# Optimization experiments

Hardware: AMD Instinct MI355X
Metric: run time of the kernel (lower is better)

## Reference

```python
import jax, jax.numpy as jnp
import numpy as np

N, E, P, D = 100000, 800000, 100000, 128

def setup_inputs() -> dict:
    key = jax.random.key(0)
    ks = jax.random.split(key, 24)
    def w(k, i, o):
        return jax.random.normal(k, (i, o), jnp.float32) * (1.0 / np.sqrt(i))
    inp = {
        'x': jax.random.normal(ks[0], (N, D), jnp.float32),
        'src': jax.random.randint(ks[1], (E,), 0, N, jnp.int32),
        'dst': jax.random.randint(ks[2], (E,), 0, N, jnp.int32),
        'pos_src': jax.random.randint(ks[3], (P,), 0, N, jnp.int32),
        'pos_dst': jax.random.randint(ks[4], (P,), 0, N, jnp.int32),
        'neg_src': jax.random.randint(ks[5], (P,), 0, N, jnp.int32),
        'neg_dst': jax.random.randint(ks[6], (P,), 0, N, jnp.int32),
        # SAGEConv params: fc_self, fc_neigh (+bias) per layer
        'Ws0': w(ks[7], D, D), 'Wn0': w(ks[8], D, D), 'b0': jnp.zeros((D,), jnp.float32),
        'Ws1': w(ks[9], D, D), 'Wn1': w(ks[10], D, D), 'b1': jnp.zeros((D,), jnp.float32),
        'Ws2': w(ks[11], D, D), 'Wn2': w(ks[12], D, D), 'b2': jnp.zeros((D,), jnp.float32),
        # predictor MLP: D->D->D->2
        'Wp0': w(ks[13], D, D), 'bp0': jnp.zeros((D,), jnp.float32),
        'Wp1': w(ks[14], D, D), 'bp1': jnp.zeros((D,), jnp.float32),
        'Wp2': w(ks[15], D, 2), 'bp2': jnp.zeros((2,), jnp.float32),
    }
    return inp

def _sage_layer(h, src, dst, n, Ws, Wn, b, act):
    # mean aggregation over in-neighbors (gather -> segment_sum -> divide)
    msum = jax.ops.segment_sum(h[src], dst, num_segments=n)      # [N, D]
    deg = jax.ops.segment_sum(jnp.ones_like(dst, jnp.float32), dst, num_segments=n)
    h_neigh = msum / jnp.maximum(deg, 1.0)[:, None]
    out = h @ Ws + h_neigh @ Wn + b
    return jax.nn.relu(out) if act else out

def _predict(hs, hd, Wp0, bp0, Wp1, bp1, Wp2, bp2):
    z = hs * hd
    z = jax.nn.relu(z @ Wp0 + bp0)
    z = jax.nn.relu(z @ Wp1 + bp1)
    return jax.nn.softmax(z @ Wp2 + bp2, axis=1)[:, 1]

def reference(x, src, dst, pos_src, pos_dst, neg_src, neg_dst,
              Ws0, Wn0, b0, Ws1, Wn1, b1, Ws2, Wn2, b2,
              Wp0, bp0, Wp1, bp1, Wp2, bp2):
    n = x.shape[0]
    h = _sage_layer(x, src, dst, n, Ws0, Wn0, b0, True)
    h = _sage_layer(h, src, dst, n, Ws1, Wn1, b1, True)
    h = _sage_layer(h, src, dst, n, Ws2, Wn2, b2, False)
    pos = _predict(h[pos_src], h[pos_dst], Wp0, bp0, Wp1, bp1, Wp2, bp2)
    neg = _predict(h[neg_src], h[neg_dst], Wp0, bp0, Wp1, bp1, Wp2, bp2)
    return (pos, neg)
```

## Files before the change

### kernel.cpp

```cpp
#include <hip/hip_runtime.h>
#include <cstdint>
#include <cstddef>
#include <cmath>

#define D 128

typedef short bf16x8 __attribute__((ext_vector_type(8)));
typedef float f32x4 __attribute__((ext_vector_type(4)));

__device__ __forceinline__ ushort f2b(float f) {
  uint x = __float_as_uint(f);
  uint r = ((x >> 16) & 1u) + 0x7fffu;
  return (ushort)((x + r) >> 16);
}
__device__ __forceinline__ float b2f(ushort u) {
  return __uint_as_float(((uint)u) << 16);
}

__global__ __launch_bounds__(256) void k_degree_p(const int* __restrict__ dst, int E,
    int* __restrict__ deg, float scale, int CE) {
  int part = blockIdx.x & 7, chunk = blockIdx.x >> 3;
  long base = (long)chunk * CE;
  for (int i = threadIdx.x; i < CE; i += 256) {
    long e = base + i;
    if (e < E) {
      int d = dst[e];
      int p = (int)((float)d * scale); if (p > 7) p = 7;
      if (p == part) atomicAdd(&deg[d], 1);
    }
  }
}

__global__ __launch_bounds__(256) void k_fill_p(const int* __restrict__ src,
    const int* __restrict__ dst, int E, int* __restrict__ cursor,
    int* __restrict__ csrc, float scale, int CE) {
  int part = blockIdx.x & 7, chunk = blockIdx.x >> 3;
  long base = (long)chunk * CE;
  for (int i = threadIdx.x; i < CE; i += 256) {
    long e = base + i;
    if (e < E) {
      int d = dst[e];
      int p = (int)((float)d * scale); if (p > 7) p = 7;
      if (p == part) {
        int s = src[e];
        int pos = atomicAdd(&cursor[d], 1);
        csrc[pos] = s;
      }
    }
  }
}

#define SCAN_T 256
#define SCAN_E 4
#define SCAN_CHUNK (SCAN_T * SCAN_E)

__global__ void k_scan_partial(const int* __restrict__ deg, int n, int* __restrict__ part) {
  __shared__ int s[SCAN_T];
  int base = blockIdx.x * SCAN_CHUNK;
  int sum = 0;
  for (int i = 0; i < SCAN_E; ++i) {
    int idx = base + (int)threadIdx.x * SCAN_E + i;
    if (idx < n) sum += deg[idx];
  }
  s[threadIdx.x] = sum; __syncthreads();
  for (int ofs = SCAN_T / 2; ofs > 0; ofs >>= 1) {
    if ((int)threadIdx.x < ofs) s[threadIdx.x] += s[threadIdx.x + ofs];
    __syncthreads();
  }
  if (threadIdx.x == 0) part[blockIdx.x] = s[0];
}

__global__ void k_scan_part_ex(int* __restrict__ part, int nb) {
  __shared__ int s[1024];
  int v = ((int)threadIdx.x < nb) ? part[threadIdx.x] : 0;
  s[threadIdx.x] = v; __syncthreads();
  for (int ofs = 1; ofs < 1024; ofs <<= 1) {
    int t = ((int)threadIdx.x >= ofs) ? s[threadIdx.x - ofs] : 0;
    __syncthreads();
    s[threadIdx.x] += t;
    __syncthreads();
  }
  if ((int)threadIdx.x < nb) part[threadIdx.x] = s[threadIdx.x] - v;
}

__global__ void k_scan_final(const int* __restrict__ deg, int n, const int* __restrict__ part,
                             int* __restrict__ rowptr, int* __restrict__ cursor, int E) {
  __shared__ int s[SCAN_T];
  int base = blockIdx.x * SCAN_CHUNK;
  int v[SCAN_E]; int local = 0;
  for (int i = 0; i < SCAN_E; ++i) {
    int idx = base + (int)threadIdx.x * SCAN_E + i;
    v[i] = (idx < n) ? deg[idx] : 0;
    local += v[i];
  }
  s[threadIdx.x] = local; __syncthreads();
  for (int ofs = 1; ofs < SCAN_T; ofs <<= 1) {
    int t = ((int)threadIdx.x >= ofs) ? s[threadIdx.x - ofs] : 0;
    __syncthreads();
    s[threadIdx.x] += t;
    __syncthreads();
  }
  int run = part[blockIdx.x] + s[threadIdx.x] - local;
  for (int i = 0; i < SCAN_E; ++i) {
    int idx = base + (int)threadIdx.x * SCAN_E + i;
    if (idx < n) { rowptr[idx] = run; cursor[idx] = run; }
    run += v[i];
  }
  if (blockIdx.x == 0 && threadIdx.x == 0) rowptr[n] = E;
}

__global__ void k_conv_bf16(const float* __restrict__ in, ushort* __restrict__ out, int n8) {
  int i = blockIdx.x * 256 + threadIdx.x;
  if (i >= n8) return;
  float4 a = ((const float4*)in)[i * 2];
  float4 b = ((const float4*)in)[i * 2 + 1];
  ushort4 o0 = {f2b(a.x), f2b(a.y), f2b(a.z), f2b(a.w)};
  ushort4 o1 = {f2b(b.x), f2b(b.y), f2b(b.z), f2b(b.w)};
  ((ushort4*)out)[i * 2] = o0;
  ((ushort4*)out)[i * 2 + 1] = o1;
}

__global__ void k_pack_all(
    const float* __restrict__ Ws0, const float* __restrict__ Wn0,
    const float* __restrict__ Ws1, const float* __restrict__ Wn1,
    const float* __restrict__ Ws2, const float* __restrict__ Wn2,
    const float* __restrict__ Wp0, const float* __restrict__ Wp1,
    ushort* __restrict__ BpL0, ushort* __restrict__ BpL1, ushort* __restrict__ BpL2,
    ushort* __restrict__ BpP0, ushort* __restrict__ BpP1) {
  int o = blockIdx.x * 256 + threadIdx.x;
  const float *W0, *W1; ushort* out; int rel;
  if (o < 32768)       { W0 = Ws0; W1 = Wn0; out = BpL0; rel = o; }
  else if (o < 65536)  { W0 = Ws1; W1 = Wn1; out = BpL1; rel = o - 32768; }
  else if (o < 98304)  { W0 = Ws2; W1 = Wn2; out = BpL2; rel = o - 65536; }
  else if (o < 114688) { W0 = Wp0; W1 = Wp0; out = BpP0; rel = o - 98304; }
  else                 { W0 = Wp1; W1 = Wp1; out = BpP1; rel = o - 114688; }
  int j = rel & 7, lane = (rel >> 3) & 63, t = (rel >> 9) & 7, ks = rel >> 12;
  int k = ks * 32 + ((lane >> 4) * 8) + j;
  int n = t * 16 + (lane & 15);
  const float* W = (k < 128) ? W0 : W1;
  int kk = (k < 128) ? k : k - 128;
  out[rel] = f2b(W[(size_t)kk * D + n]);
}

#define SMS 136
__global__ __launch_bounds__(256) void k_sage_fused(
    const ushort* __restrict__ A, const int* __restrict__ rowptr,
    const int* __restrict__ csrc, const ushort* __restrict__ Bp,
    const float* __restrict__ bias, ushort* __restrict__ out, int N, int do_relu) {
  __shared__ __align__(16) ushort smean[64][SMS];
  int tid = threadIdx.x, wave = tid >> 6, lane = tid & 63;
  int m = lane & 15, kg = lane >> 4;
  int g = tid >> 4, sub = tid & 15;
  const ushort* hb = A + sub * 8;
  #pragma unroll
  for (int j = 0; j < 4; ++j) {
    int r = g * 4 + j;
    int node = blockIdx.x * 64 + r;
    int beg = 0, end = 0;
    if (node < N) { beg = rowptr[node]; end = rowptr[node + 1]; }
    float f[8] = {0.f, 0.f, 0.f, 0.f, 0.f, 0.f, 0.f, 0.f};
    int i = beg;
    for (; i + 3 < end; i += 4) {
      int s0 = csrc[i], s1 = csrc[i + 1], s2 = csrc[i + 2], s3 = csrc[i + 3];
      bf16x8 v0 = *(const bf16x8*)(hb + (size_t)s0 * D);
      bf16x8 v1 = *(const bf16x8*)(hb + (size_t)s1 * D);
      bf16x8 v2 = *(const bf16x8*)(hb + (size_t)s2 * D);
      bf16x8 v3 = *(const bf16x8*)(hb + (size_t)s3 * D);
      #pragma unroll
      for (int q = 0; q < 8; ++q)
        f[q] += (b2f((ushort)v0[q]) + b2f((ushort)v1[q]))
              + (b2f((ushort)v2[q]) + b2f((ushort)v3[q]));
    }
    for (; i < end; ++i) {
      int s0 = csrc[i];
      bf16x8 v0 = *(const bf16x8*)(hb + (size_t)s0 * D);
      #pragma unroll
      for (int q = 0; q < 8; ++q) f[q] += b2f((ushort)v0[q]);
    }
    float inv = (end > beg) ? (1.0f / (float)(end - beg)) : 0.0f;
    bf16x8 o;
    #pragma unroll
    for (int q = 0; q < 8; ++q) o[q] = (short)f2b(f[q] * inv);
    *(bf16x8*)&smean[r][sub * 8] = o;
  }
  __syncthreads();
  int row0 = blockIdx.x * 64 + wave * 16;
  int ar = row0 + m; if (ar >= N) ar = N - 1;
  const ushort* a_self = A + (size_t)ar * D + kg * 8;
  f32x4 acc[8];
  #pragma unroll
  for (int t = 0; t < 8; ++t) acc[t] = f32x4{0.f, 0.f, 0.f, 0.f};
  #pragma unroll
  for (int ks = 0; ks < 8; ++ks) {
    bf16x8 af = (ks < 4) ? *(const bf16x8*)(a_self + ks * 32)
                         : *(const bf16x8*)&smean[wave * 16 + m][(ks - 4) * 32 + kg * 8];
    const ushort* bb = Bp + (size_t)ks * 4096 + lane * 8;
    #pragma unroll
    for (int t = 0; t < 8; ++t)
      acc[t] = __builtin_amdgcn_mfma_f32_16x16x32_bf16(af, *(const bf16x8*)(bb + t * 512), acc[t], 0, 0, 0);
  }
  #pragma unroll
  for (int t = 0; t < 8; ++t) {
    int c = t * 16 + m;
    float bv = bias[c];
    #pragma unroll
    for (int i = 0; i < 4; ++i) {
      int r = row0 + kg * 4 + i;
      float v = acc[t][i] + bv;
      if (do_relu) v = fmaxf(v, 0.f);
      if (r < N) out[(size_t)r * D + c] = f2b(v);
    }
  }
}

__global__ __launch_bounds__(256) void k_predict_mfma(
    const ushort* __restrict__ h,
    const int* __restrict__ ps, const int* __restrict__ pd,
    const int* __restrict__ ns, const int* __restrict__ nd,
    const ushort* __restrict__ Bp0, const float* __restrict__ bp0,
    const ushort* __restrict__ Bp1, const float* __restrict__ bp1,
    const float* __restrict__ Wp2, const float* __restrict__ bp2,
    float* __restrict__ outp, int P, int pb) {
  __shared__ __align__(16) ushort z1p[4][2048];
  int bi = blockIdx.x;
  const int* sidx; const int* didx; float* op;
  if (bi >= pb) { sidx = ns; didx = nd; op = outp + P; bi -= pb; }
  else          { sidx = ps; didx = pd; op = outp; }
  int tid = threadIdx.x;
  int wave = tid >> 6, lane = tid & 63;
  int m = lane & 15, kg = lane >> 4;
  int pair0 = bi * 64 + wave * 16;
  int prow = pair0 + m; int pr = (prow < P) ? prow : P - 1;
  int si = sidx[pr], di = didx[pr];
  const ushort* hs = h + (size_t)si * D + kg * 8;
  const ushort* hd = h + (size_t)di * D + kg * 8;
  f32x4 acc[8];
  #pragma unroll
  for (int t = 0; t < 8; ++t) acc[t] = f32x4{0.f, 0.f, 0.f, 0.f};
  #pragma unroll
  for (int ks = 0; ks < 4; ++ks) {
    bf16x8 as8 = *(const bf16x8*)(hs + ks * 32);
    bf16x8 ad8 = *(const bf16x8*)(hd + ks * 32);
    bf16x8 af;
    #pragma unroll
    for (int j = 0; j < 8; ++j) {
      float p = b2f((ushort)as8[j]) * b2f((ushort)ad8[j]);
      af[j] = (short)f2b(p);
    }
    const ushort* bb = Bp0 + (size_t)ks * 4096 + lane * 8;
    #pragma unroll
    for (int t = 0; t < 8; ++t)
      acc[t] = __builtin_amdgcn_mfma_f32_16x16x32_bf16(af, *(const bf16x8*)(bb + t * 512), acc[t], 0, 0, 0);
  }
  ushort* zp = &z1p[wave][0];
  #pragma unroll
  for (int t = 0; t < 8; ++t) {
    int c = t * 16 + m;
    float bv = bp0[c];
    int ks2 = c >> 5, kg2 = (c >> 3) & 3, j2 = c & 7;
    #pragma unroll
    for (int i = 0; i < 4; ++i) {
      float v = fmaxf(acc[t][i] + bv, 0.f);
      int l2 = kg2 * 16 + kg * 4 + i;
      zp[(ks2 * 64 + l2) * 8 + j2] = f2b(v);
    }
  }
  __syncthreads();
  #pragma unroll
  for (int t = 0; t < 8; ++t) acc[t] = f32x4{0.f, 0.f, 0.f, 0.f};
  #pragma unroll
  for (int ks = 0; ks < 4; ++ks) {
    bf16x8 af = *(const bf16x8*)(zp + (ks * 64 + lane) * 8);
    const ushort* bb = Bp1 + (size_t)ks * 4096 + lane * 8;
    #pragma unroll
    for (int t = 0; t < 8; ++t)
      acc[t] = __builtin_amdgcn_mfma_f32_16x16x32_bf16(af, *(const bf16x8*)(bb + t * 512), acc[t], 0, 0, 0);
  }
  float p0[4] = {0.f, 0.f, 0.f, 0.f}, p1[4] = {0.f, 0.f, 0.f, 0.f};
  #pragma unroll
  for (int t = 0; t < 8; ++t) {
    int c = t * 16 + m;
    float bv = bp1[c];
    float wa = Wp2[(size_t)c * 2], wb = Wp2[(size_t)c * 2 + 1];
    #pragma unroll
    for (int i = 0; i < 4; ++i) {
      float z = fmaxf(acc[t][i] + bv, 0.f);
      p0[i] += z * wa;
      p1[i] += z * wb;
    }
  }
  #pragma unroll
  for (int msk = 1; msk <= 8; msk <<= 1) {
    #pragma unroll
    for (int i = 0; i < 4; ++i) {
      p0[i] += __shfl_xor(p0[i], msk);
      p1[i] += __shfl_xor(p1[i], msk);
    }
  }
  if (m == 0) {
    float c0 = bp2[0], c1 = bp2[1];
    #pragma unroll
    for (int i = 0; i < 4; ++i) {
      int r = pair0 + kg * 4 + i;
      if (r < P) {
        float l0 = p0[i] + c0, l1 = p1[i] + c1;
        op[r] = 1.0f / (1.0f + expf(l0 - l1));
      }
    }
  }
}

extern "C" void kernel_launch(void* const* d_in, const int* in_sizes, int n_in,
                              void* d_out, int out_size, void* d_ws, size_t ws_size,
                              hipStream_t stream) {
  const float* x       = (const float*)d_in[0];
  const int*   src     = (const int*)d_in[1];
  const int*   dst     = (const int*)d_in[2];
  const int*   pos_src = (const int*)d_in[3];
  const int*   pos_dst = (const int*)d_in[4];
  const int*   neg_src = (const int*)d_in[5];
  const int*   neg_dst = (const int*)d_in[6];
  const float* Ws0 = (const float*)d_in[7],  *Wn0 = (const float*)d_in[8],  *b0 = (const float*)d_in[9];
  const float* Ws1 = (const float*)d_in[10], *Wn1 = (const float*)d_in[11], *b1 = (const float*)d_in[12];
  const float* Ws2 = (const float*)d_in[13], *Wn2 = (const float*)d_in[14], *b2 = (const float*)d_in[15];
  const float* Wp0 = (const float*)d_in[16], *bp0 = (const float*)d_in[17];
  const float* Wp1 = (const float*)d_in[18], *bp1 = (const float*)d_in[19];
  const float* Wp2 = (const float*)d_in[20], *bp2 = (const float*)d_in[21];
  const int N = in_sizes[0] / D;
  const int E = in_sizes[1];
  const int P = in_sizes[3];
  float* outp = (float*)d_out;

  char* ws = (char*)d_ws;
  size_t off = 0;
  auto alloc = [&](size_t bytes) -> void* {
    void* p = ws + off;
    off += (bytes + 255) & ~(size_t)255;
    return p;
  };
  ushort* xb    = (ushort*)alloc((size_t)N * D * 2);
  ushort* h1    = (ushort*)alloc((size_t)N * D * 2);
  ushort* h2    = (ushort*)alloc((size_t)N * D * 2);
  ushort* BpL0  = (ushort*)alloc(256 * D * 2);
  ushort* BpL1  = (ushort*)alloc(256 * D * 2);
  ushort* BpL2  = (ushort*)alloc(256 * D * 2);
  ushort* BpP0  = (ushort*)alloc(128 * D * 2);
  ushort* BpP1  = (ushort*)alloc(128 * D * 2);
  int*    deg    = (int*)alloc((size_t)N * 4);
  int*    rowptr = (int*)alloc((size_t)(N + 1) * 4);
  int*    cursor = (int*)alloc((size_t)N * 4);
  int*    part   = (int*)alloc(4096);
  int*    csrc   = (int*)alloc((size_t)E * 4);
  (void)ws_size; (void)n_in; (void)out_size;

  const float pscale = 8.0f / (float)N;
  const int CB = 96;
  const int CE = (E + CB - 1) / CB;

  hipMemsetAsync(deg, 0, (size_t)N * 4, stream);
  k_degree_p<<<8 * CB, 256, 0, stream>>>(dst, E, deg, pscale, CE);
  int nb = (N + SCAN_CHUNK - 1) / SCAN_CHUNK;
  k_scan_partial<<<nb, SCAN_T, 0, stream>>>(deg, N, part);
  k_scan_part_ex<<<1, 1024, 0, stream>>>(part, nb);
  k_scan_final<<<nb, SCAN_T, 0, stream>>>(deg, N, part, rowptr, cursor, E);
  k_fill_p<<<8 * CB, 256, 0, stream>>>(src, dst, E, cursor, csrc, pscale, CE);

  int n8 = N * D / 8;
  k_conv_bf16<<<(n8 + 255) / 256, 256, 0, stream>>>(x, xb, n8);
  k_pack_all<<<512, 256, 0, stream>>>(Ws0, Wn0, Ws1, Wn1, Ws2, Wn2, Wp0, Wp1,
                                      BpL0, BpL1, BpL2, BpP0, BpP1);

  int gemb = (N + 63) / 64;
  k_sage_fused<<<gemb, 256, 0, stream>>>(xb, rowptr, csrc, BpL0, b0, h1, N, 1);
  k_sage_fused<<<gemb, 256, 0, stream>>>(h1, rowptr, csrc, BpL1, b1, h2, N, 1);
  k_sage_fused<<<gemb, 256, 0, stream>>>(h2, rowptr, csrc, BpL2, b2, xb, N, 0);

  int pb = (P + 63) / 64;
  k_predict_mfma<<<2 * pb, 256, 0, stream>>>(xb, pos_src, pos_dst, neg_src, neg_dst,
                                             BpP0, bp0, BpP1, bp1, Wp2, bp2, outp, P, pb);
}
```

Measured before the change: 468.1 us.

## Interleave neighbor gathers across four rows with cooperative rowptr/index loads

Each 16-lane group now loads the rowptr values for its four destination rows once and spreads them by shuffle. Each lane preloads up to 16 neighbor indices per row into registers, which are then broadcast by shuffle. The gather loop interleaves the four rows so more independent row loads are in flight at once, replacing the serial per-row loops and their redundant csrc loads. Rows with degree above 16 fall back to a scalar tail loop, and the interleaving adds more accumulator registers.

After: 466.1 us. No clear change (-0.4%).

```diff
diff --git a/kernel.cpp b/kernel.cpp
--- a/kernel.cpp
+++ b/kernel.cpp
@@ -151,39 +151,75 @@
   int tid = threadIdx.x, wave = tid >> 6, lane = tid & 63;
   int m = lane & 15, kg = lane >> 4;
   int g = tid >> 4, sub = tid & 15;
+  int gb = (lane >> 4) << 4;
   const ushort* hb = A + sub * 8;
+
+  int node0 = blockIdx.x * 64 + g * 4;
+  int rpv = 0;
+  if (sub < 5) { int ix = node0 + sub; if (ix > N) ix = N; rpv = rowptr[ix]; }
+  int beg[4], end[4], dd[4];
   #pragma unroll
   for (int j = 0; j < 4; ++j) {
-    int r = g * 4 + j;
-    int node = blockIdx.x * 64 + r;
-    int beg = 0, end = 0;
-    if (node < N) { beg = rowptr[node]; end = rowptr[node + 1]; }
-    float f[8] = {0.f, 0.f, 0.f, 0.f, 0.f, 0.f, 0.f, 0.f};
-    int i = beg;
-    for (; i + 3 < end; i += 4) {
-      int s0 = csrc[i], s1 = csrc[i + 1], s2 = csrc[i + 2], s3 = csrc[i + 3];
-      bf16x8 v0 = *(const bf16x8*)(hb + (size_t)s0 * D);
-      bf16x8 v1 = *(const bf16x8*)(hb + (size_t)s1 * D);
-      bf16x8 v2 = *(const bf16x8*)(hb + (size_t)s2 * D);
-      bf16x8 v3 = *(const bf16x8*)(hb + (size_t)s3 * D);
+    beg[j] = __shfl(rpv, gb + j);
+    end[j] = __shfl(rpv, gb + j + 1);
+    int dg = end[j] - beg[j];
+    dd[j] = dg < 16 ? dg : 16;
+  }
+  int idxv[4];
+  #pragma unroll
+  for (int j = 0; j < 4; ++j) {
+    int i = beg[j] + sub;
+    idxv[j] = (i < end[j]) ? csrc[i] : 0;
+  }
+
+  float f[4][8];
+  #pragma unroll
+  for (int j = 0; j < 4; ++j)
+    #pragma unroll
+    for (int q = 0; q < 8; ++q) f[j][q] = 0.f;
+
+  int maxdd = dd[0];
+  if (dd[1] > maxdd) maxdd = dd[1];
+  if (dd[2] > maxdd) maxdd = dd[2];
+  if (dd[3] > maxdd) maxdd = dd[3];
+
+  for (int e = 0; e < maxdd; e += 2) {
+    #pragma unroll
+    for (int j = 0; j < 4; ++j) {
+      int s0 = __shfl(idxv[j], gb + e);
+      int s1 = __shfl(idxv[j], gb + e + 1);
+      if (e < dd[j]) {
+        bf16x8 r0 = *(const bf16x8*)(hb + (size_t)s0 * D);
+        #pragma unroll
+        for (int q = 0; q < 8; ++q) f[j][q] += b2f((ushort)r0[q]);
+      }
+      if (e + 1 < dd[j]) {
+        bf16x8 r1 = *(const bf16x8*)(hb + (size_t)s1 * D);
+        #pragma unroll
+        for (int q = 0; q < 8; ++q) f[j][q] += b2f((ushort)r1[q]);
+      }
+    }
+  }
+  #pragma unroll
+  for (int j = 0; j < 4; ++j) {
+    for (int i = beg[j] + 16; i < end[j]; ++i) {
+      int s = csrc[i];
+      bf16x8 v = *(const bf16x8*)(hb + (size_t)s * D);
       #pragma unroll
-      for (int q = 0; q < 8; ++q)
-        f[q] += (b2f((ushort)v0[q]) + b2f((ushort)v1[q]))
-              + (b2f((ushort)v2[q]) + b2f((ushort)v3[q]));
-    }
-    for (; i < end; ++i) {
-      int s0 = csrc[i];
-      bf16x8 v0 = *(const bf16x8*)(hb + (size_t)s0 * D);
-      #pragma unroll
-      for (int q = 0; q < 8; ++q) f[q] += b2f((ushort)v0[q]);
-    }
-    float inv = (end > beg) ? (1.0f / (float)(end - beg)) : 0.0f;
+      for (int q = 0; q < 8; ++q) f[j][q] += b2f((ushort)v[q]);
+    }
+  }
+  #pragma unroll
+  for (int j = 0; j < 4; ++j) {
+    int dg = end[j] - beg[j];
+    float inv = (dg > 0) ? (1.0f / (float)dg) : 0.0f;
     bf16x8 o;
     #pragma unroll
-    for (int q = 0; q < 8; ++q) o[q] = (short)f2b(f[q] * inv);
-    *(bf16x8*)&smean[r][sub * 8] = o;
+    for (int q = 0; q < 8; ++q) o[q] = (short)f2b(f[j][q] * inv);
+    *(bf16x8*)&smean[g * 4 + j][sub * 8] = o;
   }
   __syncthreads();
+
   int row0 = blockIdx.x * 64 + wave * 16;
   int ar = row0 + m; if (ar >= N) ar = N - 1;
   const ushort* a_self = A + (size_t)ar * D + kg * 8;
```

## Split fused SAGE layer into separate aggregation and MFMA GEMM kernels

Applied to the files above, without the earlier changes.

Each SAGE layer previously ran as one kernel in which every block gathered and averaged neighbours for 64 nodes into shared memory and then ran the MFMA GEMM. It now runs as two kernels. A dedicated aggregation kernel assigns one 16-lane group per node, loads up to 16 edge indices cooperatively and broadcasts them with shuffles, and writes the neighbour means to a new global buffer. A separate GEMM kernel then reads the self and neighbour rows from global memory. This is meant to give the gather more parallelism and occupancy and to remove the block-wide sync, at the cost of an extra N×D bf16 round trip through global memory and three more launches.

Result: no change. 463.8 us (-0.9%).

```diff
diff --git a/kernel.cpp b/kernel.cpp
--- a/kernel.cpp
+++ b/kernel.cpp
@@ -142,58 +142,66 @@
   out[rel] = f2b(W[(size_t)kk * D + n]);
 }
 
-#define SMS 136
-__global__ __launch_bounds__(256) void k_sage_fused(
-    const ushort* __restrict__ A, const int* __restrict__ rowptr,
-    const int* __restrict__ csrc, const ushort* __restrict__ Bp,
-    const float* __restrict__ bias, ushort* __restrict__ out, int N, int do_relu) {
-  __shared__ __align__(16) ushort smean[64][SMS];
-  int tid = threadIdx.x, wave = tid >> 6, lane = tid & 63;
-  int m = lane & 15, kg = lane >> 4;
-  int g = tid >> 4, sub = tid & 15;
-  const ushort* hb = A + sub * 8;
-  #pragma unroll
-  for (int j = 0; j < 4; ++j) {
-    int r = g * 4 + j;
-    int node = blockIdx.x * 64 + r;
-    int beg = 0, end = 0;
-    if (node < N) { beg = rowptr[node]; end = rowptr[node + 1]; }
-    float f[8] = {0.f, 0.f, 0.f, 0.f, 0.f, 0.f, 0.f, 0.f};
-    int i = beg;
-    for (; i + 3 < end; i += 4) {
-      int s0 = csrc[i], s1 = csrc[i + 1], s2 = csrc[i + 2], s3 = csrc[i + 3];
-      bf16x8 v0 = *(const bf16x8*)(hb + (size_t)s0 * D);
-      bf16x8 v1 = *(const bf16x8*)(hb + (size_t)s1 * D);
-      bf16x8 v2 = *(const bf16x8*)(hb + (size_t)s2 * D);
-      bf16x8 v3 = *(const bf16x8*)(hb + (size_t)s3 * D);
+__global__ __launch_bounds__(256) void k_aggregate2(const ushort* __restrict__ h,
+    const int* __restrict__ rowptr, const int* __restrict__ csrc,
+    ushort* __restrict__ hn, int N) {
+  int tid = threadIdx.x, lane = tid & 63;
+  int wid = (int)((blockIdx.x * 256 + tid) >> 6);
+  int g = lane >> 4, sub = lane & 15, gb = g << 4;
+  int node = wid * 4 + g;
+  if (node >= N) return;
+  int beg = rowptr[node], end = rowptr[node + 1];
+  int dg = end - beg;
+  int dd = dg < 16 ? dg : 16;
+  int i0 = beg + sub;
+  int idxv = (i0 < end) ? csrc[i0] : 0;
+  const ushort* hb = h + sub * 8;
+  float f[8] = {0.f, 0.f, 0.f, 0.f, 0.f, 0.f, 0.f, 0.f};
+  for (int e = 0; e < dd; e += 2) {
+    int s0 = __shfl(idxv, gb + e);
+    int s1 = __shfl(idxv, gb + e + 1);
+    bf16x8 r0 = *(const bf16x8*)(hb + (size_t)s0 * D);
+    if (e + 1 < dd) {
+      bf16x8 r1 = *(const bf16x8*)(hb + (size_t)s1 * D);
       #pragma unroll
       for (int q = 0; q < 8; ++q)
-        f[q] += (b2f((ushort)v0[q]) + b2f((ushort)v1[q]))
-              + (b2f((ushort)v2[q]) + b2f((ushort)v3[q]));
-    }
-    for (; i < end; ++i) {
-      int s0 = csrc[i];
-      bf16x8 v0 = *(const bf16x8*)(hb + (size_t)s0 * D);
+        f[q] += b2f((ushort)r0[q]) + b2f((ushort)r1[q]);
+    } else {
       #pragma unroll
-      for (int q = 0; q < 8; ++q) f[q] += b2f((ushort)v0[q]);
-    }
-    float inv = (end > beg) ? (1.0f / (float)(end - beg)) : 0.0f;
-    bf16x8 o;
-    #pragma unroll
-    for (int q = 0; q < 8; ++q) o[q] = (short)f2b(f[q] * inv);
-    *(bf16x8*)&smean[r][sub * 8] = o;
-  }
-  __syncthreads();
+      for (int q = 0; q < 8; ++q) f[q] += b2f((ushort)r0[q]);
+    }
+  }
+  for (int i = beg + 16; i < end; ++i) {
+    int s = csrc[i];
+    bf16x8 v = *(const bf16x8*)(hb + (size_t)s * D);
+    #pragma unroll
+    for (int q = 0; q < 8; ++q) f[q] += b2f((ushort)v[q]);
+  }
+  float inv = (dg > 0) ? (1.0f / (float)dg) : 0.0f;
+  bf16x8 o;
+  #pragma unroll
+  for (int q = 0; q < 8; ++q) o[q] = (short)f2b(f[q] * inv);
+  *(bf16x8*)(hn + (size_t)node * D + sub * 8) = o;
+}
+
+__global__ __launch_bounds__(256) void k_gemm_mfma(
+    const ushort* __restrict__ A, const ushort* __restrict__ An,
+    const ushort* __restrict__ Bp, const float* __restrict__ bias,
+    ushort* __restrict__ out, int N, int do_relu) {
+  int tid = threadIdx.x;
+  int wave = tid >> 6, lane = tid & 63;
+  int m = lane & 15, kg = lane >> 4;
   int row0 = blockIdx.x * 64 + wave * 16;
   int ar = row0 + m; if (ar >= N) ar = N - 1;
-  const ushort* a_self = A + (size_t)ar * D + kg * 8;
+  const ushort* a_self = A  + (size_t)ar * D + kg * 8;
+  const ushort* a_nei  = An + (size_t)ar * D + kg * 8;
   f32x4 acc[8];
   #pragma unroll
   for (int t = 0; t < 8; ++t) acc[t] = f32x4{0.f, 0.f, 0.f, 0.f};
   #pragma unroll
   for (int ks = 0; ks < 8; ++ks) {
-    bf16x8 af = (ks < 4) ? *(const bf16x8*)(a_self + ks * 32)
-                         : *(const bf16x8*)&smean[wave * 16 + m][(ks - 4) * 32 + kg * 8];
+    const ushort* ap = (ks < 4) ? a_self : a_nei;
+    bf16x8 af = *(const bf16x8*)(ap + (ks & 3) * 32);
     const ushort* bb = Bp + (size_t)ks * 4096 + lane * 8;
     #pragma unroll
     for (int t = 0; t < 8; ++t)
@@ -341,6 +349,7 @@
   ushort* xb    = (ushort*)alloc((size_t)N * D * 2);
   ushort* h1    = (ushort*)alloc((size_t)N * D * 2);
   ushort* h2    = (ushort*)alloc((size_t)N * D * 2);
+  ushort* hn    = (ushort*)alloc((size_t)N * D * 2);
   ushort* BpL0  = (ushort*)alloc(256 * D * 2);
   ushort* BpL1  = (ushort*)alloc(256 * D * 2);
   ushort* BpL2  = (ushort*)alloc(256 * D * 2);
@@ -370,10 +379,14 @@
   k_pack_all<<<512, 256, 0, stream>>>(Ws0, Wn0, Ws1, Wn1, Ws2, Wn2, Wp0, Wp1,
                                       BpL0, BpL1, BpL2, BpP0, BpP1);
 
+  int aggb = (N + 15) / 16;
   int gemb = (N + 63) / 64;
-  k_sage_fused<<<gemb, 256, 0, stream>>>(xb, rowptr, csrc, BpL0, b0, h1, N, 1);
-  k_sage_fused<<<gemb, 256, 0, stream>>>(h1, rowptr, csrc, BpL1, b1, h2, N, 1);
-  k_sage_fused<<<gemb, 256, 0, stream>>>(h2, rowptr, csrc, BpL2, b2, xb, N, 0);
+  k_aggregate2<<<aggb, 256, 0, stream>>>(xb, rowptr, csrc, hn, N);
+  k_gemm_mfma<<<gemb, 256, 0, stream>>>(xb, hn, BpL0, b0, h1, N, 1);
+  k_aggregate2<<<aggb, 256, 0, stream>>>(h1, rowptr, csrc, hn, N);
+  k_gemm_mfma<<<gemb, 256, 0, stream>>>(h1, hn, BpL1, b1, h2, N, 1);
+  k_aggregate2<<<aggb, 256, 0, stream>>>(h2, rowptr, csrc, hn, N);
+  k_gemm_mfma<<<gemb, 256, 0, stream>>>(h2, hn, BpL2, b2, xb, N, 0);
 
   int pb = (P + 63) / 64;
   k_predict_mfma<<<2 * pb, 256, 0, stream>>>(xb, pos_src, pos_dst, neg_src, neg_dst,
```
